# Kernel tuning notes

Hardware: AMD Instinct MI355X
Metric: run time of the kernel (lower is better)

The kernel has to match this reference:

```python
import jax, jax.numpy as jnp
import numpy as np

DIM = 384
DIM_HEAD = 32
HEADS = DIM // DIM_HEAD  # 12
INNER = HEADS * DIM_HEAD  # 384
WSZ = 8
WSZ2 = 8
SCALE = DIM_HEAD ** -0.5


def setup_inputs() -> dict:
    key = jax.random.key(0)
    k1, k2, k3, k4 = jax.random.split(key, 4)
    B, H, W = 32, 64, 64
    x = jax.random.normal(k1, (B, H, W, DIM), dtype=jnp.float32)
    # 1x1 convs == dense matrices over the channel dim
    w_qkv = jax.random.normal(k2, (DIM, 3 * INNER), dtype=jnp.float32) * (DIM ** -0.5)
    w_out = jax.random.normal(k3, (INNER, DIM), dtype=jnp.float32) * (INNER ** -0.5)
    b_out = jax.random.normal(k4, (DIM,), dtype=jnp.float32) * 0.02
    return {"x": x, "w_qkv": w_qkv, "w_out": w_out, "b_out": b_out}


def reference(x, w_qkv, w_out, b_out):
    B, H, W, D = x.shape
    nh, nw = H // WSZ, W // WSZ2
    S = WSZ * WSZ2  # tokens per window
    # 'short' attention: partition into non-overlapping wsz x wsz2 windows
    xw = (x.reshape(B, nh, WSZ, nw, WSZ2, D)
           .transpose(0, 1, 3, 2, 4, 5)
           .reshape(B * nh * nw, S, D))  # [N, S, D]
    qkv = xw @ w_qkv  # [N, S, 3*INNER] (1x1 conv, no bias)
    q, k, v = jnp.split(qkv, 3, axis=-1)
    def split_heads(t):
        N = t.shape[0]
        return t.reshape(N, S, HEADS, DIM_HEAD).transpose(0, 2, 1, 3)  # [N, h, S, d]
    q, k, v = map(split_heads, (q, k, v))
    sim = jnp.einsum('nhid,nhjd->nhij', q * SCALE, k)  # [N, h, S, S]
    attn = jax.nn.softmax(sim, axis=-1)
    out = jnp.einsum('nhij,nhjd->nhid', attn, v)  # [N, h, S, d]
    out = out.transpose(0, 2, 1, 3).reshape(-1, S, INNER)  # [N, S, INNER]
    out = out @ w_out + b_out  # 1x1 conv with bias -> [N, S, D]
    # undo windowing back to [B, H, W, D]
    out = (out.reshape(B, nh, nw, WSZ, WSZ2, D)
              .transpose(0, 1, 3, 2, 4, 5)
              .reshape(B, H, W, D))
    return out
```

## Files before the change

### kernel.cpp

```cpp
#include <hip/hip_runtime.h>

typedef _Float16 f16;
typedef _Float16 f16x4 __attribute__((ext_vector_type(4)));
typedef _Float16 f16x8 __attribute__((ext_vector_type(8)));
typedef float f32x4 __attribute__((ext_vector_type(4)));

#define MFMA_F16(A, B, C) __builtin_amdgcn_mfma_f32_16x16x32_f16(A, B, C, 0, 0, 0)

static constexpr int ROWS = 32 * 64 * 64;
static constexpr float SCALE = 0.17677669529663687f;

static constexpr size_t WQKVT_OFF = 0;
static constexpr size_t WOUTT_OFF = (size_t)1152 * 384 * 2;
static constexpr size_t QKV_OFF   = WOUTT_OFF + (size_t)384 * 384 * 2;
static constexpr size_t WS_NEEDED = QKV_OFF + (size_t)ROWS * 1152 * 2;

__global__ __launch_bounds__(256) void k_prep(const float* __restrict__ wqkv,
                                              const float* __restrict__ wout,
                                              f16* __restrict__ wqkvT,
                                              f16* __restrict__ woutT) {
  int idx = blockIdx.x * 256 + threadIdx.x;
  if (idx < 1152 * 384) {
    int c = idx / 384, k = idx - c * 384;
    wqkvT[idx] = (f16)wqkv[k * 1152 + c];
  } else {
    int i = idx - 1152 * 384;
    if (i < 384 * 384) {
      int c = i / 384, k = i - c * 384;
      woutT[i] = (f16)wout[k * 384 + c];
    }
  }
}

__global__ __launch_bounds__(256) void k_qkv(const float* __restrict__ X,
                                             const f16* __restrict__ Wt,
                                             f16* __restrict__ qkv) {
  __shared__ f16 smem[2 * 128 * 72];
  f16* As = smem;
  f16* Bs = smem + 128 * 72;

  const int tid = threadIdx.x;
  const int id = blockIdx.x;
  const int s = id & 7, t = id >> 3;
  const int n0 = (t % 9) * 128;
  const int m0 = (s * 128 + t / 9) * 128;

  const int lane = tid & 63, wave = tid >> 6;
  const int lane15 = lane & 15, quad = lane >> 4;
  const int wm = (wave >> 1) * 64, wn = (wave & 1) * 64;

  f32x4 acc[4][4] = {};
  for (int ks = 0; ks < 384; ks += 64) {
#pragma unroll
    for (int l = 0; l < 8; ++l) {
      int idx = l * 256 + tid;
      int row = idx >> 4, c4 = (idx & 15) * 4;
      float4 xv = *(const float4*)&X[(size_t)(m0 + row) * 384 + ks + c4];
      f16x4 hv;
      hv[0] = (f16)xv.x; hv[1] = (f16)xv.y; hv[2] = (f16)xv.z; hv[3] = (f16)xv.w;
      *(f16x4*)&As[row * 72 + c4] = hv;
    }
#pragma unroll
    for (int l = 0; l < 4; ++l) {
      int idx = l * 256 + tid;
      int nr = idx >> 3, c8 = (idx & 7) * 8;
      *(f16x8*)&Bs[nr * 72 + c8] = *(const f16x8*)&Wt[(size_t)(n0 + nr) * 384 + ks + c8];
    }
    __syncthreads();
#pragma unroll
    for (int kk = 0; kk < 64; kk += 32) {
      f16x8 af[4], bf[4];
#pragma unroll
      for (int i = 0; i < 4; ++i)
        af[i] = *(const f16x8*)&As[(wm + i * 16 + lane15) * 72 + kk + quad * 8];
#pragma unroll
      for (int j = 0; j < 4; ++j)
        bf[j] = *(const f16x8*)&Bs[(wn + j * 16 + lane15) * 72 + kk + quad * 8];
#pragma unroll
      for (int i = 0; i < 4; ++i)
#pragma unroll
        for (int j = 0; j < 4; ++j)
          acc[i][j] = MFMA_F16(af[i], bf[j], acc[i][j]);
    }
    __syncthreads();
  }
  f16* Cs = smem;
#pragma unroll
  for (int i = 0; i < 4; ++i)
#pragma unroll
    for (int j = 0; j < 4; ++j)
#pragma unroll
      for (int v = 0; v < 4; ++v)
        Cs[(wm + i * 16 + quad * 4 + v) * 136 + wn + j * 16 + lane15] = (f16)acc[i][j][v];
  __syncthreads();
#pragma unroll
  for (int l = 0; l < 8; ++l) {
    int idx = l * 256 + tid;
    int row = idx >> 4, c8 = (idx & 15) * 8;
    *(f16x8*)&qkv[(size_t)(m0 + row) * 1152 + n0 + c8] = *(const f16x8*)&Cs[row * 136 + c8];
  }
}

__global__ __launch_bounds__(256) void k_attn(const f16* __restrict__ qkv,
                                              const f16* __restrict__ woutT,
                                              const float* __restrict__ b_out,
                                              float* __restrict__ out) {
  __shared__ f16 vt[32 * 72];
  __shared__ f16 Pw[4][16 * 72];
  __shared__ f16 ao[64 * 392];

  const int tid = threadIdx.x;
  const int lane = tid & 63, wave = tid >> 6;
  const int lane15 = lane & 15, quad = lane >> 4;

  const int blk = blockIdx.x;
  const int b = blk >> 6, rem = blk & 63, wh = rem >> 3, ww = rem & 7;
  const int base = b * 4096 + wh * 512 + ww * 8;

  const int tq = wave * 16 + lane15;
  const size_t rowq = (size_t)(base + (tq >> 3) * 64 + (tq & 7)) * 1152;
  size_t rowk[4];
#pragma unroll
  for (int tj = 0; tj < 4; ++tj) {
    int tk = tj * 16 + lane15;
    rowk[tj] = (size_t)(base + (tk >> 3) * 64 + (tk & 7)) * 1152;
  }
  const int vt_t = tid >> 2, vt_d8 = (tid & 3) * 8;
  const size_t rowv = (size_t)(base + (vt_t >> 3) * 64 + (vt_t & 7)) * 1152;

#pragma unroll 1
  for (int h = 0; h < 12; ++h) {
    const int hoff = h * 32;
    f16x8 vv = *(const f16x8*)&qkv[rowv + 768 + hoff + vt_d8];
#pragma unroll
    for (int j = 0; j < 8; ++j) vt[(vt_d8 + j) * 72 + vt_t] = vv[j];
    __syncthreads();

    f16x8 aq = *(const f16x8*)&qkv[rowq + hoff + quad * 8];
    f32x4 sim[4];
#pragma unroll
    for (int tj = 0; tj < 4; ++tj) {
      f16x8 bk = *(const f16x8*)&qkv[rowk[tj] + 384 + hoff + quad * 8];
      f32x4 z = {};
      sim[tj] = MFMA_F16(aq, bk, z);
    }
#pragma unroll
    for (int tj = 0; tj < 4; ++tj)
#pragma unroll
      for (int v = 0; v < 4; ++v) sim[tj][v] *= SCALE;

    float pv[4][4];
#pragma unroll
    for (int v = 0; v < 4; ++v) {
      float m = fmaxf(fmaxf(sim[0][v], sim[1][v]), fmaxf(sim[2][v], sim[3][v]));
#pragma unroll
      for (int off = 1; off < 16; off <<= 1) m = fmaxf(m, __shfl_xor(m, off));
      float ssum = 0.f;
#pragma unroll
      for (int tj = 0; tj < 4; ++tj) {
        pv[tj][v] = __expf(sim[tj][v] - m);
        ssum += pv[tj][v];
      }
#pragma unroll
      for (int off = 1; off < 16; off <<= 1) ssum += __shfl_xor(ssum, off);
      float inv = 1.0f / ssum;
#pragma unroll
      for (int tj = 0; tj < 4; ++tj) pv[tj][v] *= inv;
    }
#pragma unroll
    for (int tj = 0; tj < 4; ++tj)
#pragma unroll
      for (int v = 0; v < 4; ++v)
        Pw[wave][(quad * 4 + v) * 72 + tj * 16 + lane15] = (f16)pv[tj][v];
    __syncthreads();

    f32x4 o[2] = {};
#pragma unroll
    for (int kk = 0; kk < 64; kk += 32) {
      f16x8 pa = *(const f16x8*)&Pw[wave][lane15 * 72 + kk + quad * 8];
#pragma unroll
      for (int tj = 0; tj < 2; ++tj) {
        f16x8 bvv = *(const f16x8*)&vt[(tj * 16 + lane15) * 72 + kk + quad * 8];
        o[tj] = MFMA_F16(pa, bvv, o[tj]);
      }
    }
#pragma unroll
    for (int tj = 0; tj < 2; ++tj)
#pragma unroll
      for (int v = 0; v < 4; ++v)
        ao[(wave * 16 + quad * 4 + v) * 392 + hoff + tj * 16 + lane15] = (f16)o[tj][v];
    __syncthreads();
  }

  const int n0 = wave * 96;
  float biasv[6];
#pragma unroll
  for (int tj = 0; tj < 6; ++tj) biasv[tj] = b_out[n0 + tj * 16 + lane15];
  f32x4 acc[4][6] = {};
  for (int ksi = 0; ksi < 12; ++ksi) {
    const int ks = ksi * 32;
    f16x8 af[4];
#pragma unroll
    for (int ti = 0; ti < 4; ++ti)
      af[ti] = *(const f16x8*)&ao[(ti * 16 + lane15) * 392 + ks + quad * 8];
#pragma unroll
    for (int tj = 0; tj < 6; ++tj) {
      f16x8 bf = *(const f16x8*)&woutT[(size_t)(n0 + tj * 16 + lane15) * 384 + ks + quad * 8];
#pragma unroll
      for (int ti = 0; ti < 4; ++ti) acc[ti][tj] = MFMA_F16(af[ti], bf, acc[ti][tj]);
    }
  }
#pragma unroll
  for (int ti = 0; ti < 4; ++ti)
#pragma unroll
    for (int v = 0; v < 4; ++v) {
      int t = ti * 16 + quad * 4 + v;
      size_t row = (size_t)(base + (t >> 3) * 64 + (t & 7)) * 384;
#pragma unroll
      for (int tj = 0; tj < 6; ++tj)
        out[row + n0 + tj * 16 + lane15] = acc[ti][tj][v] + biasv[tj];
    }
}

extern "C" void kernel_launch(void* const* d_in, const int* in_sizes, int n_in,
                              void* d_out, int out_size, void* d_ws, size_t ws_size,
                              hipStream_t stream) {
  const float* x = (const float*)d_in[0];
  const float* w_qkv = (const float*)d_in[1];
  const float* w_out = (const float*)d_in[2];
  const float* b_out = (const float*)d_in[3];
  float* out = (float*)d_out;

  if (ws_size < WS_NEEDED) return;

  char* ws = (char*)d_ws;
  f16* wqkvT = (f16*)(ws + WQKVT_OFF);
  f16* woutT = (f16*)(ws + WOUTT_OFF);
  f16* qkv = (f16*)(ws + QKV_OFF);

  hipLaunchKernelGGL(k_prep, dim3(2304), dim3(256), 0, stream, w_qkv, w_out, wqkvT, woutT);
  hipLaunchKernelGGL(k_qkv, dim3(9216), dim3(256), 0, stream, x, wqkvT, qkv);
  hipLaunchKernelGGL(k_attn, dim3(2048), dim3(256), 0, stream, qkv, woutT, b_out, out);
}
```

Before: 760.3 us.

## Double-buffer QKV GEMM A tile and load B fragments directly into registers

The QKV projection GEMM now prefetches the next K-slice of X into registers and writes it to a second LDS buffer while MFMAs run on the current one, so only one barrier is needed per K step. The weight operand no longer goes through shared memory: each wave loads its B fragments straight from global memory into registers, also prefetched one step ahead. This aims to hide global load latency and cut LDS traffic, at the cost of more registers (xv plus two sets of B fragments) and possibly lower occupancy.

Result: slower. 826.4 us (+8.7%).

```diff
diff --git a/kernel.cpp b/kernel.cpp
--- a/kernel.cpp
+++ b/kernel.cpp
@@ -35,9 +35,7 @@
 __global__ __launch_bounds__(256) void k_qkv(const float* __restrict__ X,
                                              const f16* __restrict__ Wt,
                                              f16* __restrict__ qkv) {
-  __shared__ f16 smem[2 * 128 * 72];
-  f16* As = smem;
-  f16* Bs = smem + 128 * 72;
+  __shared__ f16 As[2][128 * 72];
 
   const int tid = threadIdx.x;
   const int id = blockIdx.x;
@@ -49,42 +47,75 @@
   const int lane15 = lane & 15, quad = lane >> 4;
   const int wm = (wave >> 1) * 64, wn = (wave & 1) * 64;
 
+  const int arow = tid >> 4;
+  const int ac4 = (tid & 15) * 4;
+
+  const f16* bp[4];
+#pragma unroll
+  for (int j = 0; j < 4; ++j)
+    bp[j] = Wt + (size_t)(n0 + wn + j * 16 + lane15) * 384 + quad * 8;
+
+  float4 xv[8];
+  f16x8 bf[2][2][4];
+
+#pragma unroll
+  for (int l = 0; l < 8; ++l)
+    xv[l] = *(const float4*)&X[(size_t)(m0 + l * 16 + arow) * 384 + ac4];
+#pragma unroll
+  for (int kk = 0; kk < 2; ++kk)
+#pragma unroll
+    for (int j = 0; j < 4; ++j)
+      bf[0][kk][j] = *(const f16x8*)(bp[j] + kk * 32);
+#pragma unroll
+  for (int l = 0; l < 8; ++l) {
+    f16x4 hv;
+    hv[0] = (f16)xv[l].x; hv[1] = (f16)xv[l].y; hv[2] = (f16)xv[l].z; hv[3] = (f16)xv[l].w;
+    *(f16x4*)&As[0][(l * 16 + arow) * 72 + ac4] = hv;
+  }
+  __syncthreads();
+
   f32x4 acc[4][4] = {};
-  for (int ks = 0; ks < 384; ks += 64) {
-#pragma unroll
-    for (int l = 0; l < 8; ++l) {
-      int idx = l * 256 + tid;
-      int row = idx >> 4, c4 = (idx & 15) * 4;
-      float4 xv = *(const float4*)&X[(size_t)(m0 + row) * 384 + ks + c4];
-      f16x4 hv;
-      hv[0] = (f16)xv.x; hv[1] = (f16)xv.y; hv[2] = (f16)xv.z; hv[3] = (f16)xv.w;
-      *(f16x4*)&As[row * 72 + c4] = hv;
-    }
-#pragma unroll
-    for (int l = 0; l < 4; ++l) {
-      int idx = l * 256 + tid;
-      int nr = idx >> 3, c8 = (idx & 7) * 8;
-      *(f16x8*)&Bs[nr * 72 + c8] = *(const f16x8*)&Wt[(size_t)(n0 + nr) * 384 + ks + c8];
-    }
-    __syncthreads();
-#pragma unroll
-    for (int kk = 0; kk < 64; kk += 32) {
-      f16x8 af[4], bf[4];
+#pragma unroll
+  for (int ksi = 0; ksi < 6; ++ksi) {
+    const int cur = ksi & 1, nxt = cur ^ 1;
+    const int ks = ksi * 64;
+
+    if (ksi < 5) {
+#pragma unroll
+      for (int l = 0; l < 8; ++l)
+        xv[l] = *(const float4*)&X[(size_t)(m0 + l * 16 + arow) * 384 + ks + 64 + ac4];
+#pragma unroll
+      for (int kk = 0; kk < 2; ++kk)
+#pragma unroll
+        for (int j = 0; j < 4; ++j)
+          bf[nxt][kk][j] = *(const f16x8*)(bp[j] + ks + 64 + kk * 32);
+    }
+
+#pragma unroll
+    for (int kk = 0; kk < 2; ++kk) {
+      f16x8 af[4];
 #pragma unroll
       for (int i = 0; i < 4; ++i)
-        af[i] = *(const f16x8*)&As[(wm + i * 16 + lane15) * 72 + kk + quad * 8];
-#pragma unroll
-      for (int j = 0; j < 4; ++j)
-        bf[j] = *(const f16x8*)&Bs[(wn + j * 16 + lane15) * 72 + kk + quad * 8];
+        af[i] = *(const f16x8*)&As[cur][(wm + i * 16 + lane15) * 72 + kk * 32 + quad * 8];
 #pragma unroll
       for (int i = 0; i < 4; ++i)
 #pragma unroll
         for (int j = 0; j < 4; ++j)
-          acc[i][j] = MFMA_F16(af[i], bf[j], acc[i][j]);
-    }
-    __syncthreads();
-  }
-  f16* Cs = smem;
+          acc[i][j] = MFMA_F16(af[i], bf[cur][kk][j], acc[i][j]);
+    }
+
+    if (ksi < 5) {
+#pragma unroll
+      for (int l = 0; l < 8; ++l) {
+        f16x4 hv;
+        hv[0] = (f16)xv[l].x; hv[1] = (f16)xv[l].y; hv[2] = (f16)xv[l].z; hv[3] = (f16)xv[l].w;
+        *(f16x4*)&As[nxt][(l * 16 + arow) * 72 + ac4] = hv;
+      }
+    }
+    __syncthreads();
+  }
+
+  f16* Cs = (f16*)As;
 #pragma unroll
   for (int i = 0; i < 4; ++i)
 #pragma unroll
```

## Pre-convert X to fp16 and double-buffer QKV GEMM via direct global-to-LDS loads

Applied to the files above, without the earlier changes.

Adds a separate kernel that converts X to fp16 once, storing it in the output buffer as scratch. The QKV GEMM then stages A and B tiles with global_load_lds into a double-buffered, XOR-swizzled shared-memory layout, prefetching the next K slice while computing the current one. This removes the per-tile fp32-to-fp16 conversion that the GEMM previously repeated for every N-tile, and overlaps loads with MFMA work. In exchange it adds an extra pass over X, writing and rereading a 100MB fp16 copy, and uses more LDS per block.

Measured after the change: 753.8 us. Within noise of the previous version (-0.9%).

```diff
diff --git a/kernel.cpp b/kernel.cpp
--- a/kernel.cpp
+++ b/kernel.cpp
@@ -6,6 +6,10 @@
 typedef float f32x4 __attribute__((ext_vector_type(4)));
 
 #define MFMA_F16(A, B, C) __builtin_amdgcn_mfma_f32_16x16x32_f16(A, B, C, 0, 0, 0)
+#define GLDS16(gp, lp)                                                        \
+  __builtin_amdgcn_global_load_lds(                                           \
+      (const __attribute__((address_space(1))) void*)(gp),                    \
+      (__attribute__((address_space(3))) void*)(lp), 16, 0, 0)
 
 static constexpr int ROWS = 32 * 64 * 64;
 static constexpr float SCALE = 0.17677669529663687f;
@@ -32,12 +36,23 @@
   }
 }
 
-__global__ __launch_bounds__(256) void k_qkv(const float* __restrict__ X,
-                                             const f16* __restrict__ Wt,
-                                             f16* __restrict__ qkv) {
-  __shared__ f16 smem[2 * 128 * 72];
-  f16* As = smem;
-  f16* Bs = smem + 128 * 72;
+__global__ __launch_bounds__(256) void k_cvt(const float* __restrict__ X,
+                                             f16* __restrict__ Xh) {
+  int idx = blockIdx.x * 256 + threadIdx.x;
+#pragma unroll
+  for (int i = 0; i < 12; ++i) {
+    size_t j = (size_t)(idx + i * 1048576) * 4;
+    float4 v = *(const float4*)&X[j];
+    f16x4 h;
+    h[0] = (f16)v.x; h[1] = (f16)v.y; h[2] = (f16)v.z; h[3] = (f16)v.w;
+    *(f16x4*)&Xh[j] = h;
+  }
+}
+
+__global__ __launch_bounds__(256, 2) void k_qkv(const f16* __restrict__ Xh,
+                                                const f16* __restrict__ Wt,
+                                                f16* __restrict__ qkv) {
+  __shared__ __align__(16) f16 smem[4][128 * 64];
 
   const int tid = threadIdx.x;
   const int id = blockIdx.x;
@@ -49,42 +64,59 @@
   const int lane15 = lane & 15, quad = lane >> 4;
   const int wm = (wave >> 1) * 64, wn = (wave & 1) * 64;
 
+  const int r8 = lane >> 3, g7 = lane & 7;
+  const int sg = ((g7 ^ r8) << 3);
+  const f16* asrc[4];
+  const f16* bsrc[4];
+#pragma unroll
+  for (int l = 0; l < 4; ++l) {
+    asrc[l] = Xh + (size_t)(m0 + (wave * 4 + l) * 8 + r8) * 384 + sg;
+    bsrc[l] = Wt + (size_t)(n0 + (wave * 4 + l) * 8 + r8) * 384 + sg;
+  }
+
+#define STAGE(buf, ks)                                                      \
+  do {                                                                      \
+    _Pragma("unroll") for (int l = 0; l < 4; ++l)                           \
+        GLDS16(asrc[l] + (ks), &smem[(buf)][(wave * 4 + l) * 512]);         \
+    _Pragma("unroll") for (int l = 0; l < 4; ++l)                           \
+        GLDS16(bsrc[l] + (ks), &smem[2 + (buf)][(wave * 4 + l) * 512]);     \
+  } while (0)
+
+#define LDSOFF(row, kk) ((row) * 64 + ((((kk) * 4 + quad) ^ ((row) & 7)) << 3))
+
   f32x4 acc[4][4] = {};
-  for (int ks = 0; ks < 384; ks += 64) {
-#pragma unroll
-    for (int l = 0; l < 8; ++l) {
-      int idx = l * 256 + tid;
-      int row = idx >> 4, c4 = (idx & 15) * 4;
-      float4 xv = *(const float4*)&X[(size_t)(m0 + row) * 384 + ks + c4];
-      f16x4 hv;
-      hv[0] = (f16)xv.x; hv[1] = (f16)xv.y; hv[2] = (f16)xv.z; hv[3] = (f16)xv.w;
-      *(f16x4*)&As[row * 72 + c4] = hv;
-    }
-#pragma unroll
-    for (int l = 0; l < 4; ++l) {
-      int idx = l * 256 + tid;
-      int nr = idx >> 3, c8 = (idx & 7) * 8;
-      *(f16x8*)&Bs[nr * 72 + c8] = *(const f16x8*)&Wt[(size_t)(n0 + nr) * 384 + ks + c8];
-    }
-    __syncthreads();
-#pragma unroll
-    for (int kk = 0; kk < 64; kk += 32) {
+
+  STAGE(0, 0);
+  __syncthreads();
+
+#pragma unroll
+  for (int ti = 0; ti < 6; ++ti) {
+    const int cur = ti & 1;
+    if (ti < 5) STAGE(cur ^ 1, (ti + 1) * 64);
+    __builtin_amdgcn_sched_barrier(0);
+
+#pragma unroll
+    for (int kk = 0; kk < 2; ++kk) {
       f16x8 af[4], bf[4];
 #pragma unroll
       for (int i = 0; i < 4; ++i)
-        af[i] = *(const f16x8*)&As[(wm + i * 16 + lane15) * 72 + kk + quad * 8];
+        af[i] = *(const f16x8*)&smem[cur][LDSOFF(wm + i * 16 + lane15, kk)];
 #pragma unroll
       for (int j = 0; j < 4; ++j)
-        bf[j] = *(const f16x8*)&Bs[(wn + j * 16 + lane15) * 72 + kk + quad * 8];
+        bf[j] = *(const f16x8*)&smem[2 + cur][LDSOFF(wn + j * 16 + lane15, kk)];
 #pragma unroll
       for (int i = 0; i < 4; ++i)
 #pragma unroll
         for (int j = 0; j < 4; ++j)
           acc[i][j] = MFMA_F16(af[i], bf[j], acc[i][j]);
     }
-    __syncthreads();
-  }
-  f16* Cs = smem;
+
+    __syncthreads();
+  }
+#undef STAGE
+#undef LDSOFF
+
+  f16* Cs = (f16*)smem;
 #pragma unroll
   for (int i = 0; i < 4; ++i)
 #pragma unroll
@@ -237,8 +269,10 @@
   f16* wqkvT = (f16*)(ws + WQKVT_OFF);
   f16* woutT = (f16*)(ws + WOUTT_OFF);
   f16* qkv = (f16*)(ws + QKV_OFF);
+  f16* Xh = (f16*)d_out;
 
   hipLaunchKernelGGL(k_prep, dim3(2304), dim3(256), 0, stream, w_qkv, w_out, wqkvT, woutT);
-  hipLaunchKernelGGL(k_qkv, dim3(9216), dim3(256), 0, stream, x, wqkvT, qkv);
+  hipLaunchKernelGGL(k_cvt, dim3(4096), dim3(256), 0, stream, x, Xh);
+  hipLaunchKernelGGL(k_qkv, dim3(9216), dim3(256), 0, stream, Xh, wqkvT, qkv);
   hipLaunchKernelGGL(k_attn, dim3(2048), dim3(256), 0, stream, qkv, woutT, b_out, out);
 }
```
